# Performance work log

Measured on AMD Instinct MI355X. Metric: run time of the kernel, lower is better.

Reference implementation:

```python
import jax, jax.numpy as jnp
import numpy as np
from jax import lax

PB = 128          # fixed per-box patch footprint (HxW)
PATCH_HW = 256    # learned patch resolution
TV_MULT = 0.5     # patch_loss_multiplier
EPS = 1e-12       # avoids NaN at zero TV differences (original filters NaNs post-hoc)


def setup_inputs() -> dict:
    key = jax.random.key(0)
    k0, k1, k2, k3, k4 = jax.random.split(key, 5)
    B, H, W, N = 8, 1024, 1024, 16
    images = jax.random.uniform(k0, (B, H, W, 3), jnp.float32)
    gradients = jax.random.normal(k1, (B, H, W, 3), jnp.float32)
    patch = jax.random.uniform(k2, (PATCH_HW, PATCH_HW, 3), jnp.float32)
    box_yx = jax.random.randint(k3, (B, N, 2), 0, H - PB).astype(jnp.int32)
    decisions = jax.random.randint(k4, (B, N, 3), 0, 2).astype(jnp.int32)
    return {"images": images, "gradients": gradients, "patch": patch,
            "box_yx": box_yx, "decisions": decisions}


def _tv_loss(p):
    # TF: sum(sqrt((p - front)^2 + (p - down)^2)) * mult
    front = jnp.concatenate([p[:, 1:], p[:, -1:]], axis=1)
    down = jnp.concatenate([p[1:, :], p[-1:, :]], axis=0)
    return jnp.sum(jnp.sqrt((p - front) ** 2 + (p - down) ** 2 + EPS)) * TV_MULT


def reference(images, gradients, patch, box_yx, decisions):
    B, H, W, C = images.shape
    N = box_yx.shape[1]

    # ---- Patcher: resize patch -> rot90/flip per decisions -> scatter-set into images ----
    small = jax.image.resize(patch, (PB, PB, C), method="bilinear")

    def fwd_transform(d):  # d: int32[3]
        im = small
        im = jnp.where(d[0] > 0, jnp.rot90(im, k=1, axes=(0, 1)), im)
        im = jnp.where(d[1] > 0, im[:, ::-1], im)  # flip_left_right
        im = jnp.where(d[2] > 0, im[::-1], im)     # flip_up_down
        return im

    tiles = jax.vmap(jax.vmap(fwd_transform))(decisions)          # [B,N,PB,PB,C]
    tiles_f = tiles.reshape(B * N, PB, PB, C)
    b_idx = jnp.repeat(jnp.arange(B, dtype=jnp.int32), N)
    yx_f = box_yx.reshape(B * N, 2)

    def paste(imgs, xs):
        tile, b, y, x = xs
        return lax.dynamic_update_slice(imgs, tile[None], (b, y, x, jnp.int32(0))), None

    patched, _ = lax.scan(paste, images, (tiles_f, b_idx, yx_f[:, 0], yx_f[:, 1]))

    # ---- GradientProcessor: gather grads per box -> inverse transforms -> resize -> sum ----
    dec_f = decisions.reshape(B * N, 3)

    def gather_transform(b, yx, d):
        g = lax.dynamic_slice(gradients, (b, yx[0], yx[1], jnp.int32(0)), (1, PB, PB, C))[0]
        g = jnp.where(d[2] > 0, g[::-1], g)      # flip_up_down
        g = jnp.where(d[1] > 0, g[:, ::-1], g)   # flip_left_right
        g = jnp.where(d[0] > 0, jnp.rot90(g, k=3, axes=(0, 1)), g)
        return jax.image.resize(g, (PATCH_HW, PATCH_HW, C), method="bilinear")

    per_box = jax.vmap(gather_transform)(b_idx, yx_f, dec_f)      # [B*N,256,256,C]
    agg = jnp.sum(per_box, axis=0)

    # add TV-loss gradient w.r.t. patch (GradientTape in original)
    agg = agg + jax.grad(_tv_loss)(patch)
    return patched, agg
```

## Files before the change

### kernel.cpp

```cpp
#include <hip/hip_runtime.h>
#include <math.h>

#define PB    128
#define PHW   256
#define IMG_H 1024
#define IMG_W 1024
#define NBOX  16
#define NB    8
#define EPSF  1e-12f

__global__ void k_downsample(const float* __restrict__ patch, float* __restrict__ small) {
    int t = blockIdx.x * blockDim.x + threadIdx.x;
    if (t >= PB * PB * 3) return;
    int c    = t % 3;
    int rest = t / 3;
    int jl   = rest % PB;
    int il   = rest / PB;
    float sy = 2.f * il + 0.5f;
    float sx = 2.f * jl + 0.5f;
    float wy[4], wx[4];
    int   iy[4], ix[4];
    int ny = 0, nx = 0;
    float wys = 0.f, wxs = 0.f;
    #pragma unroll
    for (int d = -1; d <= 2; ++d) {
        int y = 2 * il + d;
        if (y >= 0 && y < PHW) {
            float w = 1.f - 0.5f * fabsf(sy - (float)y);
            iy[ny] = y; wy[ny] = w; wys += w; ++ny;
        }
        int x = 2 * jl + d;
        if (x >= 0 && x < PHW) {
            float w = 1.f - 0.5f * fabsf(sx - (float)x);
            ix[nx] = x; wx[nx] = w; wxs += w; ++nx;
        }
    }
    float acc = 0.f;
    for (int a = 0; a < ny; ++a) {
        float rowa = 0.f;
        for (int b2 = 0; b2 < nx; ++b2)
            rowa += wx[b2] * patch[(iy[a] * PHW + ix[b2]) * 3 + c];
        acc += wy[a] * rowa;
    }
    small[t] = acc / (wys * wxs);
}

__global__ void k_patched(const float* __restrict__ images, const float* __restrict__ small,
                          const int* __restrict__ box_yx, const int* __restrict__ dec,
                          float* __restrict__ out) {
    int b   = blockIdx.y;
    int tid = threadIdx.x;
    __shared__ int sby[NBOX], sbx[NBOX], sd0[NBOX], sd1[NBOX], sd2[NBOX];
    if (tid < NBOX) {
        sby[tid] = box_yx[(b * NBOX + tid) * 2 + 0];
        sbx[tid] = box_yx[(b * NBOX + tid) * 2 + 1];
        sd0[tid] = dec[(b * NBOX + tid) * 3 + 0];
        sd1[tid] = dec[(b * NBOX + tid) * 3 + 1];
        sd2[tid] = dec[(b * NBOX + tid) * 3 + 2];
    }
    __syncthreads();
    size_t imgbase = (size_t)b * (IMG_H * IMG_W * 3);
    const float4* in4  = (const float4*)(images + imgbase);
    float4*       out4 = (float4*)(out + imgbase);
    int q = blockIdx.x * blockDim.x + tid;
    float4 v = in4[q];
    float vv[4] = {v.x, v.y, v.z, v.w};
    int e0 = q * 4;
    #pragma unroll
    for (int k = 0; k < 4; ++k) {
        int e   = e0 + k;
        int y   = e / (IMG_W * 3);
        int rem = e - y * (IMG_W * 3);
        int x   = rem / 3;
        int c   = rem - x * 3;
        for (int n = NBOX - 1; n >= 0; --n) {
            int py = y - sby[n], px = x - sbx[n];
            if ((unsigned)py < (unsigned)PB && (unsigned)px < (unsigned)PB) {
                int i = py, j = px;
                if (sd2[n] > 0) i = PB - 1 - i;
                if (sd1[n] > 0) j = PB - 1 - j;
                int si, sj;
                if (sd0[n] > 0) { si = j; sj = PB - 1 - i; }
                else            { si = i; sj = j; }
                vv[k] = small[(si * PB + sj) * 3 + c];
                break;
            }
        }
    }
    out4[q] = make_float4(vv[0], vv[1], vv[2], vv[3]);
}

__global__ void k_sgrad(const float* __restrict__ gradients, const int* __restrict__ box_yx,
                        const int* __restrict__ dec, float* __restrict__ s_part, int ngroups) {
    int g = blockIdx.y;
    int t = blockIdx.x * blockDim.x + threadIdx.x;
    if (t >= PB * PB * 3) return;
    int c    = t % 3;
    int rest = t / 3;
    int j    = rest % PB;
    int i    = rest / PB;
    int boxes_per = (NB * NBOX) / ngroups;
    float acc = 0.f;
    for (int m = 0; m < boxes_per; ++m) {
        int box = g * boxes_per + m;
        int b   = box >> 4;
        int by = box_yx[box * 2 + 0];
        int bx = box_yx[box * 2 + 1];
        int d0 = dec[box * 3 + 0];
        int d1 = dec[box * 3 + 1];
        int d2 = dec[box * 3 + 2];
        int ii = i, jj = j;
        if (d0 > 0) { int ti = PB - 1 - jj; int tj = ii; ii = ti; jj = tj; }
        if (d1 > 0) jj = PB - 1 - jj;
        if (d2 > 0) ii = PB - 1 - ii;
        const float* gb = gradients + (size_t)b * (IMG_H * IMG_W * 3);
        acc += gb[((by + ii) * IMG_W + (bx + jj)) * 3 + c];
    }
    s_part[(size_t)g * (PB * PB * 3) + t] = acc;
}

__global__ void k_reduce(const float* __restrict__ s_part, float* __restrict__ S, int ngroups) {
    int t = blockIdx.x * blockDim.x + threadIdx.x;
    if (t >= PB * PB * 3) return;
    float a = 0.f;
    for (int g = 0; g < ngroups; ++g) a += s_part[(size_t)g * (PB * PB * 3) + t];
    S[t] = a;
}

__global__ void k_final(const float* __restrict__ S, const float* __restrict__ patch,
                        float* __restrict__ agg) {
    int t = blockIdx.x * blockDim.x + threadIdx.x;
    if (t >= PHW * PHW * 3) return;
    int c    = t % 3;
    int rest = t / 3;
    int v    = rest % PHW;
    int u    = rest / PHW;

    float fy = 0.5f * u - 0.25f;
    float fx = 0.5f * v - 0.25f;
    int i0 = (int)floorf(fy);
    int j0 = (int)floorf(fx);
    float wy[2], wx[2];
    int   iy[2], jx[2];
    int ny = 0, nx = 0;
    float wys = 0.f, wxs = 0.f;
    #pragma unroll
    for (int d = 0; d < 2; ++d) {
        int i = i0 + d;
        if (i >= 0 && i < PB) {
            float w = 1.f - fabsf(fy - (float)i);
            iy[ny] = i; wy[ny] = w; wys += w; ++ny;
        }
        int jj = j0 + d;
        if (jj >= 0 && jj < PB) {
            float w = 1.f - fabsf(fx - (float)jj);
            jx[nx] = jj; wx[nx] = w; wxs += w; ++nx;
        }
    }
    float acc = 0.f;
    for (int a = 0; a < ny; ++a)
        for (int b2 = 0; b2 < nx; ++b2)
            acc += wy[a] * wx[b2] * S[(iy[a] * PB + jx[b2]) * 3 + c];
    acc /= (wys * wxs);

    #define PAT(a, b) patch[((a) * PHW + (b)) * 3 + c]
    float p  = PAT(u, v);
    float dx = (v < PHW - 1) ? (p - PAT(u, v + 1)) : 0.f;
    float dy = (u < PHW - 1) ? (p - PAT(u + 1, v)) : 0.f;
    float r  = sqrtf(dx * dx + dy * dy + EPSF);
    float gsum = (dx + dy) / r;
    if (v > 0) {
        float pl  = PAT(u, v - 1);
        float dxl = pl - p;
        float dyl = (u < PHW - 1) ? (pl - PAT(u + 1, v - 1)) : 0.f;
        gsum -= dxl / sqrtf(dxl * dxl + dyl * dyl + EPSF);
    }
    if (u > 0) {
        float pu_ = PAT(u - 1, v);
        float dyu = pu_ - p;
        float dxu = (v < PHW - 1) ? (pu_ - PAT(u - 1, v + 1)) : 0.f;
        gsum -= dyu / sqrtf(dxu * dxu + dyu * dyu + EPSF);
    }
    #undef PAT
    agg[t] = acc + 0.5f * gsum;
}

extern "C" void kernel_launch(void* const* d_in, const int* in_sizes, int n_in,
                              void* d_out, int out_size, void* d_ws, size_t ws_size,
                              hipStream_t stream) {
    const float* images    = (const float*)d_in[0];
    const float* gradients = (const float*)d_in[1];
    const float* patch     = (const float*)d_in[2];
    const int*   box_yx    = (const int*)d_in[3];
    const int*   dec       = (const int*)d_in[4];

    float* out     = (float*)d_out;
    float* agg_out = out + (size_t)NB * IMG_H * IMG_W * 3;

    const size_t TILE = PB * PB * 3;
    int ngroups = 8;
    size_t need = TILE * (size_t)(1 + 8 + 1) * sizeof(float);
    if (ws_size < need) ngroups = 1;

    float* small  = (float*)d_ws;
    float* s_part = small + TILE;
    float* S      = s_part + (size_t)ngroups * TILE;

    hipLaunchKernelGGL(k_downsample, dim3(192), dim3(256), 0, stream, patch, small);
    hipLaunchKernelGGL(k_sgrad, dim3(192, ngroups), dim3(256), 0, stream,
                       gradients, box_yx, dec, s_part, ngroups);
    hipLaunchKernelGGL(k_reduce, dim3(192), dim3(256), 0, stream, s_part, S, ngroups);
    hipLaunchKernelGGL(k_patched, dim3((IMG_H * IMG_W * 3) / 4 / 256, NB), dim3(256), 0, stream,
                       images, small, box_yx, dec, out);
    hipLaunchKernelGGL(k_final, dim3((PHW * PHW * 3) / 256), dim3(256), 0, stream,
                       S, patch, agg_out);
}
```

Before: 298.5 us.

## Split patched output into bulk copy plus per-box paste; fold reduction into final

Replaces the per-element box-search kernel with a plain float4 copy of all images followed by a per-box paste kernel. The paste kernel skips pixels that a later box overwrites, so last-writer-wins order is kept. Drops the separate reduce kernel by summing the group partials inside the final resize kernel, and raises the group count to 16 when workspace allows. The cost targeted is the 16-box search per pixel across the whole image. In exchange, the paste adds a second write pass over box regions and the final kernel does redundant partial-sum reads.

Measured after the change: 283.3 us. 5.1% less time.

```diff
diff --git a/kernel.cpp b/kernel.cpp
--- a/kernel.cpp
+++ b/kernel.cpp
@@ -45,49 +45,46 @@
     small[t] = acc / (wys * wxs);
 }
 
-__global__ void k_patched(const float* __restrict__ images, const float* __restrict__ small,
-                          const int* __restrict__ box_yx, const int* __restrict__ dec,
-                          float* __restrict__ out) {
-    int b   = blockIdx.y;
-    int tid = threadIdx.x;
-    __shared__ int sby[NBOX], sbx[NBOX], sd0[NBOX], sd1[NBOX], sd2[NBOX];
-    if (tid < NBOX) {
-        sby[tid] = box_yx[(b * NBOX + tid) * 2 + 0];
-        sbx[tid] = box_yx[(b * NBOX + tid) * 2 + 1];
-        sd0[tid] = dec[(b * NBOX + tid) * 3 + 0];
-        sd1[tid] = dec[(b * NBOX + tid) * 3 + 1];
-        sd2[tid] = dec[(b * NBOX + tid) * 3 + 2];
-    }
-    __syncthreads();
-    size_t imgbase = (size_t)b * (IMG_H * IMG_W * 3);
-    const float4* in4  = (const float4*)(images + imgbase);
-    float4*       out4 = (float4*)(out + imgbase);
-    int q = blockIdx.x * blockDim.x + tid;
-    float4 v = in4[q];
-    float vv[4] = {v.x, v.y, v.z, v.w};
-    int e0 = q * 4;
-    #pragma unroll
-    for (int k = 0; k < 4; ++k) {
-        int e   = e0 + k;
-        int y   = e / (IMG_W * 3);
-        int rem = e - y * (IMG_W * 3);
-        int x   = rem / 3;
-        int c   = rem - x * 3;
-        for (int n = NBOX - 1; n >= 0; --n) {
-            int py = y - sby[n], px = x - sbx[n];
-            if ((unsigned)py < (unsigned)PB && (unsigned)px < (unsigned)PB) {
-                int i = py, j = px;
-                if (sd2[n] > 0) i = PB - 1 - i;
-                if (sd1[n] > 0) j = PB - 1 - j;
-                int si, sj;
-                if (sd0[n] > 0) { si = j; sj = PB - 1 - i; }
-                else            { si = i; sj = j; }
-                vv[k] = small[(si * PB + sj) * 3 + c];
-                break;
-            }
-        }
-    }
-    out4[q] = make_float4(vv[0], vv[1], vv[2], vv[3]);
+__global__ void k_copy(const float4* __restrict__ in4, float4* __restrict__ out4) {
+    int q = blockIdx.x * blockDim.x + threadIdx.x;
+    out4[q] = in4[q];
+}
+
+__global__ void k_paste(const float* __restrict__ small, const int* __restrict__ box_yx,
+                        const int* __restrict__ dec, float* __restrict__ out) {
+    int box = blockIdx.y;
+    int i   = blockIdx.x;
+    int j   = threadIdx.x;
+    int b   = box >> 4;
+    int n   = box & (NBOX - 1);
+
+    int by = box_yx[box * 2 + 0];
+    int bx = box_yx[box * 2 + 1];
+    int y  = by + i;
+    int x  = bx + j;
+
+    int base = (b << 4);
+    for (int m = n + 1; m < NBOX; ++m) {
+        int py = y - box_yx[(base + m) * 2 + 0];
+        int px = x - box_yx[(base + m) * 2 + 1];
+        if ((unsigned)py < (unsigned)PB && (unsigned)px < (unsigned)PB) return;
+    }
+
+    int d0 = dec[box * 3 + 0];
+    int d1 = dec[box * 3 + 1];
+    int d2 = dec[box * 3 + 2];
+    int ii = i, jj = j;
+    if (d2 > 0) ii = PB - 1 - ii;
+    if (d1 > 0) jj = PB - 1 - jj;
+    int si, sj;
+    if (d0 > 0) { si = jj; sj = PB - 1 - ii; }
+    else        { si = ii; sj = jj; }
+
+    const float* s = small + (si * PB + sj) * 3;
+    float* o = out + ((size_t)b * (IMG_H * IMG_W) + (size_t)y * IMG_W + x) * 3;
+    o[0] = s[0];
+    o[1] = s[1];
+    o[2] = s[2];
 }
 
 __global__ void k_sgrad(const float* __restrict__ gradients, const int* __restrict__ box_yx,
@@ -119,16 +116,8 @@
     s_part[(size_t)g * (PB * PB * 3) + t] = acc;
 }
 
-__global__ void k_reduce(const float* __restrict__ s_part, float* __restrict__ S, int ngroups) {
-    int t = blockIdx.x * blockDim.x + threadIdx.x;
-    if (t >= PB * PB * 3) return;
-    float a = 0.f;
-    for (int g = 0; g < ngroups; ++g) a += s_part[(size_t)g * (PB * PB * 3) + t];
-    S[t] = a;
-}
-
-__global__ void k_final(const float* __restrict__ S, const float* __restrict__ patch,
-                        float* __restrict__ agg) {
+__global__ void k_final(const float* __restrict__ s_part, const float* __restrict__ patch,
+                        float* __restrict__ agg, int ngroups) {
     int t = blockIdx.x * blockDim.x + threadIdx.x;
     if (t >= PHW * PHW * 3) return;
     int c    = t % 3;
@@ -159,8 +148,13 @@
     }
     float acc = 0.f;
     for (int a = 0; a < ny; ++a)
-        for (int b2 = 0; b2 < nx; ++b2)
-            acc += wy[a] * wx[b2] * S[(iy[a] * PB + jx[b2]) * 3 + c];
+        for (int b2 = 0; b2 < nx; ++b2) {
+            int idx = (iy[a] * PB + jx[b2]) * 3 + c;
+            float sv = 0.f;
+            for (int g = 0; g < ngroups; ++g)
+                sv += s_part[(size_t)g * (PB * PB * 3) + idx];
+            acc += wy[a] * wx[b2] * sv;
+        }
     acc /= (wys * wxs);
 
     #define PAT(a, b) patch[((a) * PHW + (b)) * 3 + c]
@@ -198,20 +192,20 @@
     float* agg_out = out + (size_t)NB * IMG_H * IMG_W * 3;
 
     const size_t TILE = PB * PB * 3;
-    int ngroups = 8;
-    size_t need = TILE * (size_t)(1 + 8 + 1) * sizeof(float);
-    if (ws_size < need) ngroups = 1;
+    int ngroups = 16;
+    if (ws_size < TILE * (size_t)(1 + 16) * sizeof(float)) ngroups = 8;
+    if (ws_size < TILE * (size_t)(1 + 8)  * sizeof(float)) ngroups = 1;
 
     float* small  = (float*)d_ws;
     float* s_part = small + TILE;
-    float* S      = s_part + (size_t)ngroups * TILE;
 
     hipLaunchKernelGGL(k_downsample, dim3(192), dim3(256), 0, stream, patch, small);
     hipLaunchKernelGGL(k_sgrad, dim3(192, ngroups), dim3(256), 0, stream,
                        gradients, box_yx, dec, s_part, ngroups);
-    hipLaunchKernelGGL(k_reduce, dim3(192), dim3(256), 0, stream, s_part, S, ngroups);
-    hipLaunchKernelGGL(k_patched, dim3((IMG_H * IMG_W * 3) / 4 / 256, NB), dim3(256), 0, stream,
-                       images, small, box_yx, dec, out);
+    hipLaunchKernelGGL(k_copy, dim3((IMG_H * IMG_W * 3 * NB) / 4 / 256), dim3(256), 0, stream,
+                       (const float4*)images, (float4*)out);
+    hipLaunchKernelGGL(k_paste, dim3(PB, NB * NBOX), dim3(PB), 0, stream,
+                       small, box_yx, dec, out);
     hipLaunchKernelGGL(k_final, dim3((PHW * PHW * 3) / 256), dim3(256), 0, stream,
-                       S, patch, agg_out);
-}
+                       s_part, patch, agg_out, ngroups);
+}
```
